# Optimization experiments

Hardware: AMD Instinct MI355X
Metric: run time of the kernel (lower is better)

The kernel has to match this reference:

```python
import jax, jax.numpy as jnp
import numpy as np

B, S, D = 2, 2048, 1024
H, KV, HD = 16, 4, 64          # query heads, kv heads, head_dim
ROT = 32                        # partial rotary dim
G = H // KV                     # GQA group size
SCALE = HD ** -0.5


def _rotate_half(x):
    x1, x2 = x[..., : x.shape[-1] // 2], x[..., x.shape[-1] // 2 :]
    return jnp.concatenate((-x2, x1), axis=-1)


def setup_inputs() -> dict:
    key = jax.random.key(0)
    ks = jax.random.split(key, 8)
    hidden_states = jax.random.normal(ks[0], (B, S, D), dtype=jnp.float32)
    # real rotary tables: inv_freq over ROT//2 frequencies, duplicated halves
    inv_freq = 1.0 / (10000.0 ** (jnp.arange(0, ROT, 2, dtype=jnp.float32) / ROT))
    ang = jnp.arange(S, dtype=jnp.float32)[:, None] * inv_freq[None, :]  # [S, ROT/2]
    emb = jnp.concatenate([ang, ang], axis=-1)                           # [S, ROT]
    cos = jnp.broadcast_to(jnp.cos(emb)[None], (B, S, ROT))
    sin = jnp.broadcast_to(jnp.sin(emb)[None], (B, S, ROT))
    sd = lambda fan_in: 1.0 / np.sqrt(fan_in)
    q_w = jax.random.normal(ks[1], (D, H * HD), jnp.float32) * sd(D)
    q_b = jax.random.normal(ks[2], (H * HD,), jnp.float32) * 0.02
    k_w = jax.random.normal(ks[3], (D, KV * HD), jnp.float32) * sd(D)
    v_w = jax.random.normal(ks[4], (D, KV * HD), jnp.float32) * sd(D)
    v_b = jax.random.normal(ks[5], (KV * HD,), jnp.float32) * 0.02
    o_w = jax.random.normal(ks[6], (H * HD, D), jnp.float32) * sd(H * HD)
    o_b = jax.random.normal(ks[7], (D,), jnp.float32) * 0.02
    return {"hidden_states": hidden_states, "cos": cos, "sin": sin,
            "q_w": q_w, "q_b": q_b, "k_w": k_w, "v_w": v_w, "v_b": v_b,
            "o_w": o_w, "o_b": o_b}


def reference(hidden_states, cos, sin, q_w, q_b, k_w, v_w, v_b, o_w, o_b):
    x = hidden_states
    # projections -> [B, heads, S, HD]
    q = (x @ q_w + q_b).reshape(B, S, H, HD).transpose(0, 2, 1, 3)
    k = (x @ k_w).reshape(B, S, KV, HD).transpose(0, 2, 1, 3)
    v = (x @ v_w + v_b).reshape(B, S, KV, HD).transpose(0, 2, 1, 3)
    # partial RoPE; cos/sin broadcast over head dim
    c = cos[:, None, :, :]
    s = sin[:, None, :, :]
    q_rot, q_pass = q[..., :ROT], q[..., ROT:]
    k_rot, k_pass = k[..., :ROT], k[..., ROT:]
    q = jnp.concatenate([q_rot * c + _rotate_half(q_rot) * s, q_pass], axis=-1)
    k = jnp.concatenate([k_rot * c + _rotate_half(k_rot) * s, k_pass], axis=-1)
    # GQA without materializing repeated K/V: group queries per kv head
    qg = q.reshape(B, KV, G, S, HD)
    scores = jnp.einsum("bkgsd,bktd->bkgst", qg, k) * SCALE  # [B,KV,G,S,S]
    probs = jax.nn.softmax(scores, axis=-1)
    out = jnp.einsum("bkgst,bktd->bkgsd", probs, v)          # [B,KV,G,S,HD]
    out = out.reshape(B, H, S, HD).transpose(0, 2, 1, 3).reshape(B, S, H * HD)
    attn_output = out @ o_w + o_b
    attn_weights = probs.reshape(B, H, S, S)
    return attn_output, attn_weights
```

## Files before the change

kernel.cpp:

```cpp
#include <hip/hip_runtime.h>
#include <hip/hip_bf16.h>

typedef _Float16 f16;
typedef _Float16 f16x8 __attribute__((ext_vector_type(8)));
typedef _Float16 f16x4 __attribute__((ext_vector_type(4)));
typedef float f32x4 __attribute__((ext_vector_type(4)));

#define MFMA_F16(a, b, c) __builtin_amdgcn_mfma_f32_16x16x32_f16((a), (b), (c), 0, 0, 0)

static constexpr int S_TOK = 2048;
static constexpr int N_HEAD = 16;
static constexpr int N_KV = 4;
static constexpr int HD = 64;
static constexpr float SCL2E = 0.125f * 1.4426950408889634f;

static constexpr size_t OFF_X16 = 0;
static constexpr size_t OFF_QW = 4194304;
static constexpr size_t OFF_KW = OFF_QW + 1048576;
static constexpr size_t OFF_VW = OFF_KW + 262144;
static constexpr size_t OFF_OW = OFF_VW + 262144;
static constexpr size_t OFF_QS = OFF_OW + 1048576;
static constexpr size_t OFF_KS = OFF_QS + 4194304;
static constexpr size_t OFF_VS = OFF_KS + 1048576;
static constexpr size_t OFF_OS = OFF_VS + 1048576;
static constexpr size_t CVT_TOTAL = OFF_OW + 1048576;

__global__ __launch_bounds__(256) void k_cvt(
    const float* __restrict__ x, const float* __restrict__ qw,
    const float* __restrict__ kw, const float* __restrict__ vw,
    const float* __restrict__ ow, f16* __restrict__ dst) {
  size_t i = ((size_t)blockIdx.x * 256 + threadIdx.x) * 4;
  if (i >= CVT_TOTAL) return;
  const float* src;
  size_t off;
  if (i < OFF_QW) { src = x; off = i; }
  else if (i < OFF_KW) { src = qw; off = i - OFF_QW; }
  else if (i < OFF_VW) { src = kw; off = i - OFF_KW; }
  else if (i < OFF_OW) { src = vw; off = i - OFF_VW; }
  else { src = ow; off = i - OFF_OW; }
  float4 v = *(const float4*)(src + off);
  *(f16x4*)(dst + i) = f16x4{(f16)v.x, (f16)v.y, (f16)v.z, (f16)v.w};
}

__global__ __launch_bounds__(256) void k_qkv(
    const f16* __restrict__ x, const float* __restrict__ cosp,
    const float* __restrict__ sinp, const f16* __restrict__ q_w,
    const float* __restrict__ q_b, const f16* __restrict__ k_w,
    const f16* __restrict__ v_w, const float* __restrict__ v_b,
    f16* __restrict__ q_ws, f16* __restrict__ k_ws, f16* __restrict__ v_ws) {
  __shared__ f16 wb[64][72];
  const int tid = threadIdx.x;
  const int wave = tid >> 6, lane = tid & 63;
  const int l16 = lane & 15, g = lane >> 4;
  const int m0 = blockIdx.x * 64;
  const int n0 = blockIdx.y * 64;

  const f16* W;
  int ldW, nloc, mode;
  if (n0 < 1024) { W = q_w; ldW = 1024; nloc = n0; mode = 0; }
  else if (n0 < 1280) { W = k_w; ldW = 256; nloc = n0 - 1024; mode = 1; }
  else { W = v_w; ldW = 256; nloc = n0 - 1280; mode = 2; }

  f32x4 acc[4] = {};
  const int kk = (tid >> 4) * 4;
  const int nn = (tid & 15) * 4;

  for (int k0 = 0; k0 < 1024; k0 += 64) {
    const f16* wp = W + (size_t)(k0 + kk) * ldW + nloc + nn;
    f16x4 w0 = *(const f16x4*)(wp);
    f16x4 w1 = *(const f16x4*)(wp + ldW);
    f16x4 w2 = *(const f16x4*)(wp + 2 * ldW);
    f16x4 w3 = *(const f16x4*)(wp + 3 * ldW);
    __syncthreads();
    *(f16x4*)&wb[nn + 0][kk] = f16x4{w0[0], w1[0], w2[0], w3[0]};
    *(f16x4*)&wb[nn + 1][kk] = f16x4{w0[1], w1[1], w2[1], w3[1]};
    *(f16x4*)&wb[nn + 2][kk] = f16x4{w0[2], w1[2], w2[2], w3[2]};
    *(f16x4*)&wb[nn + 3][kk] = f16x4{w0[3], w1[3], w2[3], w3[3]};
    __syncthreads();
    const f16* xp = x + (size_t)(m0 + wave * 16 + l16) * 1024 + k0 + g * 8;
#pragma unroll
    for (int ks = 0; ks < 2; ++ks) {
      f16x8 af = *(const f16x8*)(xp + ks * 32);
#pragma unroll
      for (int n = 0; n < 4; ++n) {
        f16x8 bf = *(const f16x8*)&wb[n * 16 + l16][ks * 32 + g * 8];
        acc[n] = MFMA_F16(af, bf, acc[n]);
      }
    }
  }

  if (mode == 0) {
#pragma unroll
    for (int n = 0; n < 4; ++n) {
      float bsc = q_b[n0 + n * 16 + l16];
#pragma unroll
      for (int r = 0; r < 4; ++r) acc[n][r] += bsc;
    }
  } else if (mode == 2) {
#pragma unroll
    for (int n = 0; n < 4; ++n) {
      float bsc = v_b[nloc + n * 16 + l16];
#pragma unroll
      for (int r = 0; r < 4; ++r) acc[n][r] += bsc;
    }
  }
  if (mode < 2) {
#pragma unroll
    for (int r = 0; r < 4; ++r) {
      int row = m0 + wave * 16 + g * 4 + r;
      int bb = row >> 11, ss = row & 2047;
      float c = cosp[((size_t)bb * S_TOK + ss) * 32 + l16];
      float sn = sinp[((size_t)bb * S_TOK + ss) * 32 + l16];
      float v0 = acc[0][r], v1 = acc[1][r];
      acc[0][r] = v0 * c - v1 * sn;
      acc[1][r] = v1 * c + v0 * sn;
    }
  }
#pragma unroll
  for (int n = 0; n < 4; ++n) {
#pragma unroll
    for (int r = 0; r < 4; ++r) {
      int row = m0 + wave * 16 + g * 4 + r;
      int bb = row >> 11, ss = row & 2047;
      f16 val = (f16)acc[n][r];
      if (mode == 0) {
        int col = n0 + n * 16 + l16;
        int h = col >> 6, hd = col & 63;
        q_ws[(((size_t)bb * N_HEAD + h) * S_TOK + ss) * HD + hd] = val;
      } else {
        int col = nloc + n * 16 + l16;
        int kh = col >> 6, hd = col & 63;
        if (mode == 1)
          k_ws[(((size_t)bb * N_KV + kh) * S_TOK + ss) * HD + hd] = val;
        else
          v_ws[(((size_t)bb * N_KV + kh) * HD + hd) * S_TOK + ss] = val;
      }
    }
  }
}

__global__ __launch_bounds__(256, 3) void k_attn(
    const f16* __restrict__ q_ws, const f16* __restrict__ k_ws,
    const f16* __restrict__ v_ws, f16* __restrict__ o_ws,
    float* __restrict__ probs) {
  __shared__ f16 plds_all[4][32][72];
  __shared__ float lpart[2][2][32];
  __shared__ float osum[2][32][68];
  const int tid = threadIdx.x;
  const int wave = tid >> 6, lane = tid & 63;
  const int pairi = wave >> 1, half = wave & 1;
  const int l16 = lane & 15, g = lane >> 4;
  const int head = blockIdx.x >> 5;
  const int rt = blockIdx.x & 31;
  const int b = head >> 4, h = head & 15, kvh = h >> 2;
  const int qrow0 = rt * 64 + pairi * 32;

  const f16* qb = q_ws + ((size_t)head * S_TOK + qrow0) * HD;
  const f16* kb = k_ws + (size_t)(b * N_KV + kvh) * S_TOK * HD;
  const f16* vb = v_ws + (size_t)(b * N_KV + kvh) * HD * S_TOK;
  float* pout = probs + (size_t)head * S_TOK * S_TOK + (size_t)qrow0 * S_TOK;
  f16(*plds)[72] = plds_all[wave];

  f16x8 qf[2][2];
#pragma unroll
  for (int mf = 0; mf < 2; ++mf)
#pragma unroll
    for (int ks = 0; ks < 2; ++ks)
      qf[mf][ks] = *(const f16x8*)(qb + (mf * 16 + l16) * HD + ks * 32 + g * 8);

  const int kt0 = half * 16, kt1 = kt0 + 16;

  float lsum[2][4] = {};
  for (int kt = kt0; kt < kt1; ++kt) {
    const f16* kp = kb + (size_t)kt * 64 * HD;
#pragma unroll
    for (int n = 0; n < 4; ++n) {
      f16x8 k0f = *(const f16x8*)(kp + (n * 16 + l16) * HD + g * 8);
      f16x8 k1f = *(const f16x8*)(kp + (n * 16 + l16) * HD + 32 + g * 8);
#pragma unroll
      for (int mf = 0; mf < 2; ++mf) {
        f32x4 s = {};
        s = MFMA_F16(qf[mf][0], k0f, s);
        s = MFMA_F16(qf[mf][1], k1f, s);
#pragma unroll
        for (int r = 0; r < 4; ++r) lsum[mf][r] += exp2f(s[r] * SCL2E);
      }
    }
  }
#pragma unroll
  for (int mf = 0; mf < 2; ++mf)
#pragma unroll
    for (int r = 0; r < 4; ++r) {
      float v = lsum[mf][r];
      v += __shfl_xor(v, 1, 64);
      v += __shfl_xor(v, 2, 64);
      v += __shfl_xor(v, 4, 64);
      v += __shfl_xor(v, 8, 64);
      lsum[mf][r] = v;
    }
  if (l16 == 0) {
#pragma unroll
    for (int mf = 0; mf < 2; ++mf)
#pragma unroll
      for (int r = 0; r < 4; ++r)
        lpart[pairi][half][mf * 16 + g * 4 + r] = lsum[mf][r];
  }
  __syncthreads();
  float linv[2][4];
#pragma unroll
  for (int mf = 0; mf < 2; ++mf)
#pragma unroll
    for (int r = 0; r < 4; ++r) {
      int row = mf * 16 + g * 4 + r;
      linv[mf][r] = 1.0f / (lpart[pairi][0][row] + lpart[pairi][1][row]);
    }

  f32x4 oacc[2][4] = {};
  const int orow = lane >> 4, oq = lane & 15;
  for (int kt = kt0; kt < kt1; ++kt) {
    const f16* kp = kb + (size_t)kt * 64 * HD;
#pragma unroll
    for (int n = 0; n < 4; ++n) {
      f16x8 k0f = *(const f16x8*)(kp + (n * 16 + l16) * HD + g * 8);
      f16x8 k1f = *(const f16x8*)(kp + (n * 16 + l16) * HD + 32 + g * 8);
#pragma unroll
      for (int mf = 0; mf < 2; ++mf) {
        f32x4 s = {};
        s = MFMA_F16(qf[mf][0], k0f, s);
        s = MFMA_F16(qf[mf][1], k1f, s);
#pragma unroll
        for (int r = 0; r < 4; ++r) {
          float p = exp2f(s[r] * SCL2E) * linv[mf][r];
          plds[mf * 16 + g * 4 + r][n * 16 + l16] = (f16)p;
        }
      }
    }
    asm volatile("s_waitcnt lgkmcnt(0)" ::: "memory");
    f16x8 pa[2][2];
#pragma unroll
    for (int mf = 0; mf < 2; ++mf)
#pragma unroll
      for (int ks = 0; ks < 2; ++ks)
        pa[mf][ks] = *(const f16x8*)&plds[mf * 16 + l16][ks * 32 + g * 8];
#pragma unroll
    for (int nh = 0; nh < 4; ++nh) {
      const f16* vp = vb + (size_t)(nh * 16 + l16) * S_TOK + kt * 64;
      f16x8 v0f = *(const f16x8*)(vp + g * 8);
      f16x8 v1f = *(const f16x8*)(vp + 32 + g * 8);
#pragma unroll
      for (int mf = 0; mf < 2; ++mf) {
        oacc[mf][nh] = MFMA_F16(pa[mf][0], v0f, oacc[mf][nh]);
        oacc[mf][nh] = MFMA_F16(pa[mf][1], v1f, oacc[mf][nh]);
      }
    }
#pragma unroll
    for (int it = 0; it < 8; ++it) {
      int rr = it * 4 + orow;
      f16x4 pv = *(const f16x4*)&plds[rr][oq * 4];
      f32x4 ov = {(float)pv[0], (float)pv[1], (float)pv[2], (float)pv[3]};
      __builtin_nontemporal_store(
          ov, (f32x4*)(pout + (size_t)rr * S_TOK + kt * 64 + oq * 4));
    }
    asm volatile("" ::: "memory");
  }

  if (half == 1) {
#pragma unroll
    for (int mf = 0; mf < 2; ++mf)
#pragma unroll
      for (int nh = 0; nh < 4; ++nh)
#pragma unroll
        for (int r = 0; r < 4; ++r)
          osum[pairi][mf * 16 + g * 4 + r][nh * 16 + l16] = oacc[mf][nh][r];
  }
  __syncthreads();
  if (half == 0) {
#pragma unroll
    for (int mf = 0; mf < 2; ++mf)
#pragma unroll
      for (int nh = 0; nh < 4; ++nh)
#pragma unroll
        for (int r = 0; r < 4; ++r) {
          int row = mf * 16 + g * 4 + r;
          float v = oacc[mf][nh][r] + osum[pairi][row][nh * 16 + l16];
          o_ws[((size_t)b * S_TOK + qrow0 + row) * 1024 + h * HD + nh * 16 +
               l16] = (f16)v;
        }
  }
}

__global__ __launch_bounds__(256) void k_oproj(
    const f16* __restrict__ a, const f16* __restrict__ o_w,
    const float* __restrict__ o_b, float* __restrict__ out) {
  __shared__ f16 wb[64][72];
  const int tid = threadIdx.x;
  const int wave = tid >> 6, lane = tid & 63;
  const int l16 = lane & 15, g = lane >> 4;
  const int m0 = blockIdx.x * 64, n0 = blockIdx.y * 64;
  f32x4 acc[4] = {};
  const int kk = (tid >> 4) * 4, nn = (tid & 15) * 4;
  for (int k0 = 0; k0 < 1024; k0 += 64) {
    const f16* wp = o_w + (size_t)(k0 + kk) * 1024 + n0 + nn;
    f16x4 w0 = *(const f16x4*)(wp);
    f16x4 w1 = *(const f16x4*)(wp + 1024);
    f16x4 w2 = *(const f16x4*)(wp + 2048);
    f16x4 w3 = *(const f16x4*)(wp + 3072);
    __syncthreads();
    *(f16x4*)&wb[nn + 0][kk] = f16x4{w0[0], w1[0], w2[0], w3[0]};
    *(f16x4*)&wb[nn + 1][kk] = f16x4{w0[1], w1[1], w2[1], w3[1]};
    *(f16x4*)&wb[nn + 2][kk] = f16x4{w0[2], w1[2], w2[2], w3[2]};
    *(f16x4*)&wb[nn + 3][kk] = f16x4{w0[3], w1[3], w2[3], w3[3]};
    __syncthreads();
    const f16* ap = a + (size_t)(m0 + wave * 16 + l16) * 1024 + k0 + g * 8;
#pragma unroll
    for (int ks = 0; ks < 2; ++ks) {
      f16x8 af = *(const f16x8*)(ap + ks * 32);
#pragma unroll
      for (int n = 0; n < 4; ++n) {
        f16x8 bf = *(const f16x8*)&wb[n * 16 + l16][ks * 32 + g * 8];
        acc[n] = MFMA_F16(af, bf, acc[n]);
      }
    }
  }
#pragma unroll
  for (int n = 0; n < 4; ++n) {
    float bsc = o_b[n0 + n * 16 + l16];
#pragma unroll
    for (int r = 0; r < 4; ++r) {
      int row = m0 + wave * 16 + g * 4 + r;
      out[(size_t)row * 1024 + n0 + n * 16 + l16] = acc[n][r] + bsc;
    }
  }
}

extern "C" void kernel_launch(void* const* d_in, const int* in_sizes, int n_in,
                              void* d_out, int out_size, void* d_ws,
                              size_t ws_size, hipStream_t stream) {
  (void)in_sizes; (void)n_in; (void)out_size; (void)ws_size;
  const float* x    = (const float*)d_in[0];
  const float* cosp = (const float*)d_in[1];
  const float* sinp = (const float*)d_in[2];
  const float* q_w  = (const float*)d_in[3];
  const float* q_b  = (const float*)d_in[4];
  const float* k_w  = (const float*)d_in[5];
  const float* v_w  = (const float*)d_in[6];
  const float* v_b  = (const float*)d_in[7];
  const float* o_w  = (const float*)d_in[8];
  const float* o_b  = (const float*)d_in[9];

  f16* ws = (f16*)d_ws;
  f16* x16  = ws + OFF_X16;
  f16* qw16 = ws + OFF_QW;
  f16* kw16 = ws + OFF_KW;
  f16* vw16 = ws + OFF_VW;
  f16* ow16 = ws + OFF_OW;
  f16* q_ws = ws + OFF_QS;
  f16* k_ws = ws + OFF_KS;
  f16* v_ws = ws + OFF_VS;
  f16* o_ws = ws + OFF_OS;
  float* out = (float*)d_out;
  float* probs = out + 4194304;

  k_cvt<<<dim3((CVT_TOTAL / 4 + 255) / 256), 256, 0, stream>>>(
      x, q_w, k_w, v_w, o_w, ws);
  k_qkv<<<dim3(64, 24), 256, 0, stream>>>(x16, cosp, sinp, qw16, q_b, kw16,
                                          vw16, v_b, q_ws, k_ws, v_ws);
  k_attn<<<dim3(1024), 256, 0, stream>>>(q_ws, k_ws, v_ws, o_ws, probs);
  k_oproj<<<dim3(64, 16), 256, 0, stream>>>(o_ws, ow16, o_b, out);
}
```

Measured before the change: 298.1 us.

## Transpose attention MFMA operands so probs store directly from registers

Swaps the A/B operands of the QK and PV MFMAs so each lane holds four consecutive key columns of one query row. Probabilities are then written to global memory straight from registers as f32x4 nontemporal stores, and the old LDS readback and f16-to-f32 reconversion pass is removed. The row-sum reduction shrinks to two cross-group shuffles, and the output and partial-sum writes become vectorized. Block indices are also remapped so blocks sharing a batch and KV head are interleaved for better K/V cache reuse, and V loads are hoisted ahead of the LDS wait.

```diff
diff --git a/kernel.cpp b/kernel.cpp
--- a/kernel.cpp
+++ b/kernel.cpp
@@ -150,9 +150,12 @@
   const int wave = tid >> 6, lane = tid & 63;
   const int pairi = wave >> 1, half = wave & 1;
   const int l16 = lane & 15, g = lane >> 4;
-  const int head = blockIdx.x >> 5;
-  const int rt = blockIdx.x & 31;
-  const int b = head >> 4, h = head & 15, kvh = h >> 2;
+  const int bid = blockIdx.x;
+  const int combo = bid & 7, local = bid >> 3;
+  const int b = combo >> 2, kvh = combo & 3;
+  const int h = kvh * 4 + (local >> 5);
+  const int rt = local & 31;
+  const int head = b * N_HEAD + h;
   const int qrow0 = rt * 64 + pairi * 32;
 
   const f16* qb = q_ws + ((size_t)head * S_TOK + qrow0) * HD;
@@ -170,7 +173,7 @@
 
   const int kt0 = half * 16, kt1 = kt0 + 16;
 
-  float lsum[2][4] = {};
+  float lsum[2] = {0.0f, 0.0f};
   for (int kt = kt0; kt < kt1; ++kt) {
     const f16* kp = kb + (size_t)kt * 64 * HD;
 #pragma unroll
@@ -180,43 +183,30 @@
 #pragma unroll
       for (int mf = 0; mf < 2; ++mf) {
         f32x4 s = {};
-        s = MFMA_F16(qf[mf][0], k0f, s);
-        s = MFMA_F16(qf[mf][1], k1f, s);
-#pragma unroll
-        for (int r = 0; r < 4; ++r) lsum[mf][r] += exp2f(s[r] * SCL2E);
-      }
-    }
-  }
-#pragma unroll
-  for (int mf = 0; mf < 2; ++mf)
-#pragma unroll
-    for (int r = 0; r < 4; ++r) {
-      float v = lsum[mf][r];
-      v += __shfl_xor(v, 1, 64);
-      v += __shfl_xor(v, 2, 64);
-      v += __shfl_xor(v, 4, 64);
-      v += __shfl_xor(v, 8, 64);
-      lsum[mf][r] = v;
-    }
-  if (l16 == 0) {
-#pragma unroll
-    for (int mf = 0; mf < 2; ++mf)
-#pragma unroll
-      for (int r = 0; r < 4; ++r)
-        lpart[pairi][half][mf * 16 + g * 4 + r] = lsum[mf][r];
+        s = MFMA_F16(k0f, qf[mf][0], s);
+        s = MFMA_F16(k1f, qf[mf][1], s);
+        lsum[mf] += exp2f(s[0] * SCL2E) + exp2f(s[1] * SCL2E) +
+                    exp2f(s[2] * SCL2E) + exp2f(s[3] * SCL2E);
+      }
+    }
+  }
+#pragma unroll
+  for (int mf = 0; mf < 2; ++mf) {
+    float v = lsum[mf];
+    v += __shfl_xor(v, 16, 64);
+    v += __shfl_xor(v, 32, 64);
+    lsum[mf] = v;
+  }
+  if (g == 0) {
+    lpart[pairi][half][l16] = lsum[0];
+    lpart[pairi][half][16 + l16] = lsum[1];
   }
   __syncthreads();
-  float linv[2][4];
-#pragma unroll
-  for (int mf = 0; mf < 2; ++mf)
-#pragma unroll
-    for (int r = 0; r < 4; ++r) {
-      int row = mf * 16 + g * 4 + r;
-      linv[mf][r] = 1.0f / (lpart[pairi][0][row] + lpart[pairi][1][row]);
-    }
+  float linv[2];
+  linv[0] = 1.0f / (lpart[pairi][0][l16] + lpart[pairi][1][l16]);
+  linv[1] = 1.0f / (lpart[pairi][0][16 + l16] + lpart[pairi][1][16 + l16]);
 
   f32x4 oacc[2][4] = {};
-  const int orow = lane >> 4, oq = lane & 15;
   for (int kt = kt0; kt < kt1; ++kt) {
     const f16* kp = kb + (size_t)kt * 64 * HD;
 #pragma unroll
@@ -226,16 +216,27 @@
 #pragma unroll
       for (int mf = 0; mf < 2; ++mf) {
         f32x4 s = {};
-        s = MFMA_F16(qf[mf][0], k0f, s);
-        s = MFMA_F16(qf[mf][1], k1f, s);
-#pragma unroll
-        for (int r = 0; r < 4; ++r) {
-          float p = exp2f(s[r] * SCL2E) * linv[mf][r];
-          plds[mf * 16 + g * 4 + r][n * 16 + l16] = (f16)p;
-        }
-      }
+        s = MFMA_F16(k0f, qf[mf][0], s);
+        s = MFMA_F16(k1f, qf[mf][1], s);
+        f32x4 p;
+#pragma unroll
+        for (int r = 0; r < 4; ++r) p[r] = exp2f(s[r] * SCL2E) * linv[mf];
+        __builtin_nontemporal_store(
+            p, (f32x4*)(pout + (size_t)(mf * 16 + l16) * S_TOK + kt * 64 +
+                        n * 16 + g * 4));
+        *(f16x4*)&plds[mf * 16 + l16][n * 16 + g * 4] =
+            f16x4{(f16)p[0], (f16)p[1], (f16)p[2], (f16)p[3]};
+      }
+    }
+    f16x8 vf[4][2];
+#pragma unroll
+    for (int nh = 0; nh < 4; ++nh) {
+      const f16* vp = vb + (size_t)(nh * 16 + l16) * S_TOK + kt * 64;
+      vf[nh][0] = *(const f16x8*)(vp + g * 8);
+      vf[nh][1] = *(const f16x8*)(vp + 32 + g * 8);
     }
     asm volatile("s_waitcnt lgkmcnt(0)" ::: "memory");
+    __builtin_amdgcn_sched_barrier(0);
     f16x8 pa[2][2];
 #pragma unroll
     for (int mf = 0; mf < 2; ++mf)
@@ -243,24 +244,12 @@
       for (int ks = 0; ks < 2; ++ks)
         pa[mf][ks] = *(const f16x8*)&plds[mf * 16 + l16][ks * 32 + g * 8];
 #pragma unroll
-    for (int nh = 0; nh < 4; ++nh) {
-      const f16* vp = vb + (size_t)(nh * 16 + l16) * S_TOK + kt * 64;
-      f16x8 v0f = *(const f16x8*)(vp + g * 8);
-      f16x8 v1f = *(const f16x8*)(vp + 32 + g * 8);
-#pragma unroll
-      for (int mf = 0; mf < 2; ++mf) {
-        oacc[mf][nh] = MFMA_F16(pa[mf][0], v0f, oacc[mf][nh]);
-        oacc[mf][nh] = MFMA_F16(pa[mf][1], v1f, oacc[mf][nh]);
-      }
-    }
-#pragma unroll
-    for (int it = 0; it < 8; ++it) {
-      int rr = it * 4 + orow;
-      f16x4 pv = *(const f16x4*)&plds[rr][oq * 4];
-      f32x4 ov = {(float)pv[0], (float)pv[1], (float)pv[2], (float)pv[3]};
-      __builtin_nontemporal_store(
-          ov, (f32x4*)(pout + (size_t)rr * S_TOK + kt * 64 + oq * 4));
-    }
+    for (int mf = 0; mf < 2; ++mf)
+#pragma unroll
+      for (int nh = 0; nh < 4; ++nh) {
+        oacc[mf][nh] = MFMA_F16(vf[nh][0], pa[mf][0], oacc[mf][nh]);
+        oacc[mf][nh] = MFMA_F16(vf[nh][1], pa[mf][1], oacc[mf][nh]);
+      }
     asm volatile("" ::: "memory");
   }
 
@@ -269,23 +258,20 @@
     for (int mf = 0; mf < 2; ++mf)
 #pragma unroll
       for (int nh = 0; nh < 4; ++nh)
-#pragma unroll
-        for (int r = 0; r < 4; ++r)
-          osum[pairi][mf * 16 + g * 4 + r][nh * 16 + l16] = oacc[mf][nh][r];
+        *(f32x4*)&osum[pairi][mf * 16 + l16][nh * 16 + g * 4] = oacc[mf][nh];
   }
   __syncthreads();
   if (half == 0) {
 #pragma unroll
     for (int mf = 0; mf < 2; ++mf)
 #pragma unroll
-      for (int nh = 0; nh < 4; ++nh)
-#pragma unroll
-        for (int r = 0; r < 4; ++r) {
-          int row = mf * 16 + g * 4 + r;
-          float v = oacc[mf][nh][r] + osum[pairi][row][nh * 16 + l16];
-          o_ws[((size_t)b * S_TOK + qrow0 + row) * 1024 + h * HD + nh * 16 +
-               l16] = (f16)v;
-        }
+      for (int nh = 0; nh < 4; ++nh) {
+        f32x4 o = oacc[mf][nh] +
+                  *(const f32x4*)&osum[pairi][mf * 16 + l16][nh * 16 + g * 4];
+        f16x4 ov = {(f16)o[0], (f16)o[1], (f16)o[2], (f16)o[3]};
+        *(f16x4*)(o_ws + ((size_t)b * S_TOK + qrow0 + mf * 16 + l16) * 1024 +
+                  h * HD + nh * 16 + g * 4) = ov;
+      }
   }
 }
 
```

Measured after the change: 319.5 us. 1.07x slower.
